# Optimization experiments

Hardware: AMD Instinct MI355X
Metric: run time of the kernel (lower is better)

## Reference

```python
import jax, jax.numpy as jnp
import numpy as np

N = 100000   # nodes
E = 800000   # edges
IN = 128     # input features
HID = 128    # hidden channels (= trans out_channels, heads=1)
OUT = 64     # output classes
EPS = 1e-5
ALPHA = 0.5


def _lin(k, fi, fo):
    kw, kb = jax.random.split(k)
    w = jax.random.normal(kw, (fi, fo), jnp.float32) / np.float32(np.sqrt(fi))
    b = jax.random.normal(kb, (fo,), jnp.float32) * 0.01
    return w, b


def setup_inputs() -> dict:
    key = jax.random.key(0)
    k = jax.random.split(key, 12)
    x = jax.random.normal(k[0], (N, IN), jnp.float32)
    edge_index = jax.random.randint(k[1], (2, E), 0, N)
    edge_type = jax.random.randint(k[2], (E,), 0, 2)
    edge_weight = jax.random.uniform(k[3], (E,), jnp.float32)
    t_fc_w, t_fc_b = _lin(k[4], IN, HID)
    wq, wq_b = _lin(k[5], HID, HID)
    wk, wk_b = _lin(k[6], HID, HID)
    wv, wv_b = _lin(k[7], HID, HID)
    g_fc_w, g_fc_b = _lin(k[8], IN, HID)
    g_w1, g_b1 = _lin(k[9], HID, HID)
    g_w2, g_b2 = _lin(k[10], HID, HID)
    out_w, out_b = _lin(k[11], 2 * HID, OUT)
    ones = jnp.ones((HID,), jnp.float32)
    zeros = jnp.zeros((HID,), jnp.float32)
    return dict(
        x=x, edge_weight=edge_weight,
        t_fc_w=t_fc_w, t_fc_b=t_fc_b, t_ln0_g=ones, t_ln0_b=zeros,
        wq=wq, wq_b=wq_b, wk=wk, wk_b=wk_b, wv=wv, wv_b=wv_b,
        t_ln1_g=ones, t_ln1_b=zeros,
        g_fc_w=g_fc_w, g_fc_b=g_fc_b,
        bn0_g=ones, bn0_b=zeros, bn0_m=zeros, bn0_v=ones,
        g_w1=g_w1, g_b1=g_b1, bn1_g=ones, bn1_b=zeros, bn1_m=zeros, bn1_v=ones,
        g_w2=g_w2, g_b2=g_b2, bn2_g=ones, bn2_b=zeros, bn2_m=zeros, bn2_v=ones,
        out_w=out_w, out_b=out_b,
        edge_index=edge_index, edge_type=edge_type,
    )


def _ln(x, g, b):
    m = x.mean(-1, keepdims=True)
    v = ((x - m) ** 2).mean(-1, keepdims=True)
    return (x - m) / jnp.sqrt(v + EPS) * g + b


def _bn(x, g, b, m, v):  # eval-mode BatchNorm1d (running stats)
    return (x - m) / jnp.sqrt(v + EPS) * g + b


def _full_attn(q, k, v):
    # q:[N,H,M] k:[L,H,M] v:[L,H,D]; global (Frobenius) norm as in torch.norm(qs, p=2)
    q = q / jnp.linalg.norm(q)
    k = k / jnp.linalg.norm(k)
    n = q.shape[0]
    kvs = jnp.einsum('lhm,lhd->hmd', k, v)
    num = jnp.einsum('nhm,hmd->nhd', q, kvs) + n * v
    ksum = k.sum(0)  # [H,M]
    denom = jnp.einsum('nhm,hm->nh', q, ksum)[..., None] + n
    return num / denom


def _hetero(x, row, col, ew, mask, W, b):
    # degree over edges of this type, normalized SpMM: out[col] += val * x[row]
    d = jax.ops.segment_sum(mask.astype(jnp.float32), col, num_segments=N)
    val = ew / jnp.sqrt(d[col] * d[row])
    val = jnp.where(mask, jnp.nan_to_num(val, nan=0.0, posinf=0.0, neginf=0.0), 0.0)
    agg = jax.ops.segment_sum(val[:, None] * x[row], col, num_segments=N)
    return agg @ W + b


def reference(x, edge_weight, t_fc_w, t_fc_b, t_ln0_g, t_ln0_b, wq, wq_b, wk, wk_b,
              wv, wv_b, t_ln1_g, t_ln1_b, g_fc_w, g_fc_b, bn0_g, bn0_b, bn0_m, bn0_v,
              g_w1, g_b1, bn1_g, bn1_b, bn1_m, bn1_v, g_w2, g_b2, bn2_g, bn2_b, bn2_m,
              bn2_v, out_w, out_b, edge_index, edge_type):
    relu = jax.nn.relu
    # --- transformer (kernelized global attention) branch ---
    h = relu(_ln(x @ t_fc_w + t_fc_b, t_ln0_g, t_ln0_b))
    q = (h @ wq + wq_b)[:, None, :]   # [N,1,HID]
    kk = (h @ wk + wk_b)[:, None, :]
    vv = (h @ wv + wv_b)[:, None, :]
    z = _full_attn(q, kk, vv).mean(axis=1)
    x_trans = relu(_ln(ALPHA * z + (1.0 - ALPHA) * h, t_ln1_g, t_ln1_b))
    # --- alternating hetero GNN branch ---
    row, col = edge_index[0], edge_index[1]
    g = relu(_bn(x @ g_fc_w + g_fc_b, bn0_g, bn0_b, bn0_m, bn0_v))
    g1 = relu(_bn(_hetero(g, row, col, edge_weight, edge_type == 0, g_w1, g_b1),
                  bn1_g, bn1_b, bn1_m, bn1_v)) + g
    g2 = relu(_bn(_hetero(g1, row, col, edge_weight, edge_type == 1, g_w2, g_b2),
                  bn2_g, bn2_b, bn2_m, bn2_v)) + g1
    return jnp.tanh(jnp.concatenate([x_trans, g2], axis=1) @ out_w + out_b)
```

## Files before the change

kernel.cpp:

```cpp
#include <hip/hip_runtime.h>
#include <cmath>

#define EPSF 1e-5f

typedef __bf16 bfx8 __attribute__((ext_vector_type(8)));
typedef float  f32x4 __attribute__((ext_vector_type(4)));

__device__ __forceinline__ float4 ld4(const float* p){ return *(const float4*)p; }
__device__ __forceinline__ unsigned f2bf(float f){
    unsigned u = __builtin_bit_cast(unsigned, f);
    return (u + 0x7FFFu + ((u >> 16) & 1u)) >> 16;
}
__device__ __forceinline__ float bf2f(unsigned u){
    return __builtin_bit_cast(float, u << 16);
}
__device__ __forceinline__ bfx8 lds_ld(const char* p){ return *(const bfx8*)p; }
__device__ __forceinline__ unsigned short bf16u(float f){ return (unsigned short)f2bf(f); }

__global__ __launch_bounds__(256)
void wconv_all(const float* __restrict__ s0, const float* __restrict__ s1,
               const float* __restrict__ s2, const float* __restrict__ s3,
               const float* __restrict__ s4, const float* __restrict__ s5,
               unsigned short* __restrict__ WT)
{
    int gid   = blockIdx.x*256 + threadIdx.x;
    int seg   = gid >> 11;
    int chunk = gid & 2047;
    int ln    = chunk & 63;
    unsigned short tmp[8];
    if (seg < 5) {
        const float* s = seg==0?s0: seg==1?s1: seg==2?s2: seg==3?s3: s4;
        int nf = chunk >> 8, ks = (chunk >> 6) & 3;
        int c  = nf*16 + (ln & 15);
        int k0 = ks*32 + (ln >> 4)*8;
        #pragma unroll
        for (int j = 0; j < 8; ++j) tmp[j] = bf16u(s[(size_t)(k0+j)*128 + c]);
        *(uint4*)&WT[seg*16384 + chunk*8] = *(uint4*)tmp;
    } else {
        int nf = chunk >> 9, ks = (chunk >> 6) & 7;
        int c  = nf*16 + (ln & 15);
        int k0 = ks*32 + (ln >> 4)*8;
        #pragma unroll
        for (int j = 0; j < 8; ++j) tmp[j] = bf16u(s5[(size_t)(k0+j)*64 + c]);
        *(uint4*)&WT[5*16384 + chunk*8] = *(uint4*)tmp;
    }
}

__global__ __launch_bounds__(256)
void fused_front(const float* __restrict__ x,
                 const unsigned short* __restrict__ wt_tfc,
                 const unsigned short* __restrict__ wt_wv,
                 const unsigned short* __restrict__ wt_gfc,
                 const float* __restrict__ tfcb, const float* __restrict__ ln0g,
                 const float* __restrict__ ln0b, const float* __restrict__ wvb,
                 const float* __restrict__ ln1g, const float* __restrict__ ln1b,
                 const float* __restrict__ gfcb, const float* __restrict__ bn0g,
                 const float* __restrict__ bn0b, const float* __restrict__ bn0m,
                 const float* __restrict__ bn0v,
                 unsigned short* __restrict__ XTb, float* __restrict__ Gf,
                 unsigned short* __restrict__ Gb, int nrows)
{
    __shared__ __align__(16) char lds[81920];
    char*  Ar  = lds;
    char*  WrA = lds + 16384;
    char*  WrB = lds + 49152;
    float* Cst = (float*)WrB;
    const int tid  = threadIdx.x;
    const int row0 = blockIdx.x * 64;
    const int w  = tid >> 6, ln = tid & 63, lr = ln & 15, lg = ln >> 4;
    const int ksw = (lr & 7) << 4;

    #pragma unroll
    for (int i = 0; i < 4; ++i) {
        int c  = tid + i*256, r = c >> 4, k0 = (c & 15)*8;
        uint4 v4 = make_uint4(0,0,0,0);
        if (row0 + r < nrows) {
            float4 f0 = ld4(&x[(size_t)(row0+r)*128 + k0]);
            float4 f1 = ld4(&x[(size_t)(row0+r)*128 + k0 + 4]);
            v4.x = f2bf(f0.x) | (f2bf(f0.y) << 16);
            v4.y = f2bf(f0.z) | (f2bf(f0.w) << 16);
            v4.z = f2bf(f1.x) | (f2bf(f1.y) << 16);
            v4.w = f2bf(f1.z) | (f2bf(f1.w) << 16);
        }
        *(uint4*)&Ar[r*256 + ((k0*2) ^ ((r&7)<<4))] = v4;
    }
    #pragma unroll
    for (int i = 0; i < 8; ++i) {
        int c = tid + i*256;
        *(uint4*)&WrA[c*16] = *(const uint4*)&wt_tfc[c*8];
    }
    #pragma unroll
    for (int i = 0; i < 8; ++i) {
        int c = tid + i*256;
        *(uint4*)&WrB[c*16] = *(const uint4*)&wt_gfc[c*8];
    }
    __syncthreads();

    const char* Abase = &Ar[(w*16 + lr)*256];
    f32x4 acc[8];
    float h[8][4];

    #pragma unroll
    for (int nf = 0; nf < 8; ++nf) acc[nf] = (f32x4){0.f,0.f,0.f,0.f};
    #pragma unroll
    for (int ks = 0; ks < 4; ++ks) {
        int kb = ks*64 + lg*16;
        bfx8 a = lds_ld(Abase + (kb ^ ksw));
        #pragma unroll
        for (int nf = 0; nf < 8; ++nf) {
            bfx8 b = lds_ld(&WrA[(nf*4+ks)*1024 + ln*16]);
            acc[nf] = __builtin_amdgcn_mfma_f32_16x16x32_bf16(a, b, acc[nf], 0, 0, 0);
        }
    }
    {
        float gl[8], bl[8];
        #pragma unroll
        for (int nf = 0; nf < 8; ++nf) {
            int c = nf*16 + lr;
            gl[nf] = ln0g[c]; bl[nf] = ln0b[c];
            float bb = tfcb[c];
            #pragma unroll
            for (int i = 0; i < 4; ++i) h[nf][i] = acc[nf][i] + bb;
        }
        #pragma unroll
        for (int i = 0; i < 4; ++i) {
            float s = 0.f, s2 = 0.f;
            #pragma unroll
            for (int nf = 0; nf < 8; ++nf) { s += h[nf][i]; s2 += h[nf][i]*h[nf][i]; }
            #pragma unroll
            for (int m = 1; m < 16; m <<= 1) { s += __shfl_xor(s, m); s2 += __shfl_xor(s2, m); }
            float mean = s * (1.f/128.f);
            float inv  = rsqrtf(s2 * (1.f/128.f) - mean*mean + EPSF);
            #pragma unroll
            for (int nf = 0; nf < 8; ++nf)
                h[nf][i] = fmaxf((h[nf][i]-mean)*inv*gl[nf] + bl[nf], 0.f);
        }
    }
    #pragma unroll
    for (int nf = 0; nf < 8; ++nf) acc[nf] = (f32x4){0.f,0.f,0.f,0.f};
    #pragma unroll
    for (int ks = 0; ks < 4; ++ks) {
        int kb = ks*64 + lg*16;
        bfx8 a = lds_ld(Abase + (kb ^ ksw));
        #pragma unroll
        for (int nf = 0; nf < 8; ++nf) {
            bfx8 b = lds_ld(&WrB[(nf*4+ks)*1024 + ln*16]);
            acc[nf] = __builtin_amdgcn_mfma_f32_16x16x32_bf16(a, b, acc[nf], 0, 0, 0);
        }
    }
    #pragma unroll
    for (int nf = 0; nf < 8; ++nf) {
        int c = nf*16 + lr;
        float sc = bn0g[c] * rsqrtf(bn0v[c] + EPSF);
        float sh = bn0b[c] - bn0m[c]*sc;
        float bb = gfcb[c];
        #pragma unroll
        for (int i = 0; i < 4; ++i)
            acc[nf][i] = fmaxf((acc[nf][i] + bb)*sc + sh, 0.f);
    }
    __syncthreads();

    #pragma unroll
    for (int nf = 0; nf < 8; ++nf) {
        int c = nf*16 + lr;
        #pragma unroll
        for (int i = 0; i < 4; ++i) {
            int r = w*16 + lg*4 + i;
            Cst[r*128 + c] = acc[nf][i];
            *(unsigned short*)&Ar[(r*256 + c*2) ^ ((r&7)<<4)] = bf16u(h[nf][i]);
        }
    }
    #pragma unroll
    for (int i = 0; i < 8; ++i) {
        int c = tid + i*256;
        *(uint4*)&WrA[c*16] = *(const uint4*)&wt_wv[c*8];
    }
    __syncthreads();

    #pragma unroll
    for (int i = 0; i < 8; ++i) {
        int c = tid + i*256, r = c >> 5, k4 = (c & 31)*4;
        if (row0 + r < nrows) {
            f32x4 v = *(f32x4*)&Cst[r*128 + k4];
            *(f32x4*)&Gf[(size_t)(row0+r)*128 + k4] = v;
            uint2 pk;
            pk.x = f2bf(v[0]) | (f2bf(v[1]) << 16);
            pk.y = f2bf(v[2]) | (f2bf(v[3]) << 16);
            *(uint2*)&Gb[(size_t)(row0+r)*128 + k4] = pk;
        }
    }
    #pragma unroll
    for (int nf = 0; nf < 8; ++nf) acc[nf] = (f32x4){0.f,0.f,0.f,0.f};
    #pragma unroll
    for (int ks = 0; ks < 4; ++ks) {
        int kb = ks*64 + lg*16;
        bfx8 a = lds_ld(Abase + (kb ^ ksw));
        #pragma unroll
        for (int nf = 0; nf < 8; ++nf) {
            bfx8 b = lds_ld(&WrA[(nf*4+ks)*1024 + ln*16]);
            acc[nf] = __builtin_amdgcn_mfma_f32_16x16x32_bf16(a, b, acc[nf], 0, 0, 0);
        }
    }
    {
        float gl[8], bl[8];
        #pragma unroll
        for (int nf = 0; nf < 8; ++nf) {
            int c = nf*16 + lr;
            gl[nf] = ln1g[c]; bl[nf] = ln1b[c];
            float bb = wvb[c];
            #pragma unroll
            for (int i = 0; i < 4; ++i)
                h[nf][i] = 0.5f*(acc[nf][i] + bb) + 0.5f*h[nf][i];
        }
        #pragma unroll
        for (int i = 0; i < 4; ++i) {
            float s = 0.f, s2 = 0.f;
            #pragma unroll
            for (int nf = 0; nf < 8; ++nf) { s += h[nf][i]; s2 += h[nf][i]*h[nf][i]; }
            #pragma unroll
            for (int m = 1; m < 16; m <<= 1) { s += __shfl_xor(s, m); s2 += __shfl_xor(s2, m); }
            float mean = s * (1.f/128.f);
            float inv  = rsqrtf(s2 * (1.f/128.f) - mean*mean + EPSF);
            #pragma unroll
            for (int nf = 0; nf < 8; ++nf)
                h[nf][i] = fmaxf((h[nf][i]-mean)*inv*gl[nf] + bl[nf], 0.f);
        }
    }
    __syncthreads();

    #pragma unroll
    for (int nf = 0; nf < 8; ++nf) {
        int c = nf*16 + lr;
        #pragma unroll
        for (int i = 0; i < 4; ++i)
            Cst[(w*16 + lg*4 + i)*128 + c] = h[nf][i];
    }
    __syncthreads();
    #pragma unroll
    for (int i = 0; i < 8; ++i) {
        int c = tid + i*256, r = c >> 5, k4 = (c & 31)*4;
        if (row0 + r < nrows) {
            f32x4 v = *(f32x4*)&Cst[r*128 + k4];
            uint2 pk;
            pk.x = f2bf(v[0]) | (f2bf(v[1]) << 16);
            pk.y = f2bf(v[2]) | (f2bf(v[3]) << 16);
            *(uint2*)&XTb[(size_t)(row0+r)*128 + k4] = pk;
        }
    }
}

__global__ __launch_bounds__(256)
void mgemm(const unsigned short* __restrict__ Ab16, const unsigned short* __restrict__ WTf,
           const float* __restrict__ bias, float* __restrict__ Cf,
           unsigned short* __restrict__ Cb, int nrows,
           const float* __restrict__ p0, const float* __restrict__ p1,
           const float* __restrict__ p2, const float* __restrict__ p3,
           const float* __restrict__ resid)
{
    __shared__ __align__(16) char lds[50176];
    char*  Ar  = lds;
    char*  Wr  = lds + 16384;
    float* Cst = (float*)Wr;
    const int tid  = threadIdx.x;
    const int row0 = blockIdx.x * 64;
    const int w  = tid >> 6, ln = tid & 63, lr = ln & 15, lg = ln >> 4;
    const int ksw = (lr & 7) << 4;

    #pragma unroll
    for (int i = 0; i < 4; ++i) {
        int c  = tid + i*256, r = c >> 4, k0 = (c & 15)*8;
        uint4 v = make_uint4(0,0,0,0);
        if (row0 + r < nrows)
            v = *(const uint4*)&Ab16[(size_t)(row0+r)*128 + k0];
        *(uint4*)&Ar[r*256 + ((k0*2) ^ ((r&7)<<4))] = v;
    }
    #pragma unroll
    for (int i = 0; i < 8; ++i) {
        int c = tid + i*256;
        *(uint4*)&Wr[c*16] = *(const uint4*)&WTf[c*8];
    }
    __syncthreads();

    const char* Abase = &Ar[(w*16 + lr)*256];
    f32x4 acc[8];
    #pragma unroll
    for (int nf = 0; nf < 8; ++nf) acc[nf] = (f32x4){0.f,0.f,0.f,0.f};
    #pragma unroll
    for (int ks = 0; ks < 4; ++ks) {
        int kb = ks*64 + lg*16;
        bfx8 a = lds_ld(Abase + (kb ^ ksw));
        #pragma unroll
        for (int nf = 0; nf < 8; ++nf) {
            bfx8 b = lds_ld(&Wr[(nf*4+ks)*1024 + ln*16]);
            acc[nf] = __builtin_amdgcn_mfma_f32_16x16x32_bf16(a, b, acc[nf], 0, 0, 0);
        }
    }

    float t[8][4];
    #pragma unroll
    for (int nf = 0; nf < 8; ++nf) {
        int c = nf*16 + lr;
        float sc = p0[c] * rsqrtf(p3[c] + EPSF);
        float sh = p1[c] - p2[c]*sc;
        float bb = bias[c];
        #pragma unroll
        for (int i = 0; i < 4; ++i)
            t[nf][i] = fmaxf((acc[nf][i] + bb)*sc + sh, 0.f);
    }

    __syncthreads();
    #pragma unroll
    for (int nf = 0; nf < 8; ++nf)
        #pragma unroll
        for (int i = 0; i < 4; ++i)
            Cst[(w*16 + lg*4 + i)*132 + nf*16 + lr] = t[nf][i];
    __syncthreads();
    #pragma unroll
    for (int i = 0; i < 8; ++i) {
        int c = tid + i*256, r = c >> 5, c4 = (c & 31)*4;
        if (row0 + r >= nrows) continue;
        f32x4 v = *(f32x4*)&Cst[r*132 + c4];
        float4 rr = ld4(resid + (size_t)(row0+r)*128 + c4);
        v.x += rr.x; v.y += rr.y; v.z += rr.z; v.w += rr.w;
        *(f32x4*)&Cf[(size_t)(row0+r)*128 + c4] = v;
        uint2 pk;
        pk.x = f2bf(v.x) | (f2bf(v.y) << 16);
        pk.y = f2bf(v.z) | (f2bf(v.w) << 16);
        *(uint2*)&Cb[(size_t)(row0+r)*128 + c4] = pk;
    }
}

__global__ __launch_bounds__(256)
void mgemm_out(const unsigned short* __restrict__ Ab16,
               const unsigned short* __restrict__ WTf,
               const float* __restrict__ bias,
               const float* __restrict__ p0, const float* __restrict__ p1,
               const float* __restrict__ p2, const float* __restrict__ p3,
               const float* __restrict__ resid,
               const unsigned short* __restrict__ XTb,
               const unsigned short* __restrict__ WToutf,
               const float* __restrict__ outB,
               float* __restrict__ out, int nrows)
{
    __shared__ __align__(16) char lds[65536];
    char* Ar  = lds;
    char* Wg  = lds + 16384;
    char* WrX = lds + 16384;
    char* WrO = lds + 32768;
    const int tid  = threadIdx.x;
    const int row0 = blockIdx.x * 64;
    const int w  = tid >> 6, ln = tid & 63, lr = ln & 15, lg = ln >> 4;
    const int ksw = (lr & 7) << 4;

    #pragma unroll
    for (int i = 0; i < 4; ++i) {
        int c  = tid + i*256, r = c >> 4, k0 = (c & 15)*8;
        uint4 v = make_uint4(0,0,0,0);
        if (row0 + r < nrows)
            v = *(const uint4*)&Ab16[(size_t)(row0+r)*128 + k0];
        *(uint4*)&Ar[r*256 + ((k0*2) ^ ((r&7)<<4))] = v;
    }
    #pragma unroll
    for (int i = 0; i < 8; ++i) {
        int c = tid + i*256;
        *(uint4*)&Wg[c*16] = *(const uint4*)&WTf[c*8];
    }
    __syncthreads();

    const char* Abase = &Ar[(w*16 + lr)*256];
    f32x4 acc[8];
    #pragma unroll
    for (int nf = 0; nf < 8; ++nf) acc[nf] = (f32x4){0.f,0.f,0.f,0.f};
    #pragma unroll
    for (int ks = 0; ks < 4; ++ks) {
        int kb = ks*64 + lg*16;
        bfx8 a = lds_ld(Abase + (kb ^ ksw));
        #pragma unroll
        for (int nf = 0; nf < 8; ++nf) {
            bfx8 b = lds_ld(&Wg[(nf*4+ks)*1024 + ln*16]);
            acc[nf] = __builtin_amdgcn_mfma_f32_16x16x32_bf16(a, b, acc[nf], 0, 0, 0);
        }
    }
    float t[8][4];
    #pragma unroll
    for (int nf = 0; nf < 8; ++nf) {
        int c = nf*16 + lr;
        float sc = p0[c] * rsqrtf(p3[c] + EPSF);
        float sh = p1[c] - p2[c]*sc;
        float bb = bias[c];
        #pragma unroll
        for (int i = 0; i < 4; ++i) {
            int r = row0 + w*16 + lg*4 + i;
            float rv = (r < nrows) ? resid[(size_t)r*128 + c] : 0.f;
            t[nf][i] = fmaxf((acc[nf][i] + bb)*sc + sh, 0.f) + rv;
        }
    }
    __syncthreads();

    #pragma unroll
    for (int nf = 0; nf < 8; ++nf) {
        int c = nf*16 + lr;
        #pragma unroll
        for (int i = 0; i < 4; ++i) {
            int r = w*16 + lg*4 + i;
            *(unsigned short*)&Ar[(r*256 + c*2) ^ ((r&7)<<4)] = bf16u(t[nf][i]);
        }
    }
    #pragma unroll
    for (int i = 0; i < 4; ++i) {
        int c  = tid + i*256, r = c >> 4, k0 = (c & 15)*8;
        uint4 v = make_uint4(0,0,0,0);
        if (row0 + r < nrows)
            v = *(const uint4*)&XTb[(size_t)(row0+r)*128 + k0];
        *(uint4*)&WrX[r*256 + ((k0*2) ^ ((r&7)<<4))] = v;
    }
    #pragma unroll
    for (int i = 0; i < 8; ++i) {
        int c = tid + i*256;
        *(uint4*)&WrO[c*16] = *(const uint4*)&WToutf[c*8];
    }
    __syncthreads();

    f32x4 acc2[4];
    #pragma unroll
    for (int nf = 0; nf < 4; ++nf) acc2[nf] = (f32x4){0.f,0.f,0.f,0.f};
    const char* Xbase = &WrX[(w*16 + lr)*256];
    #pragma unroll
    for (int ks = 0; ks < 8; ++ks) {
        int kb = (ks & 3)*64 + lg*16;
        bfx8 a = (ks < 4) ? lds_ld(Xbase + (kb ^ ksw))
                          : lds_ld(Abase + (kb ^ ksw));
        #pragma unroll
        for (int nf = 0; nf < 4; ++nf) {
            bfx8 b = lds_ld(&WrO[(nf*8+ks)*1024 + ln*16]);
            acc2[nf] = __builtin_amdgcn_mfma_f32_16x16x32_bf16(a, b, acc2[nf], 0, 0, 0);
        }
    }
    #pragma unroll
    for (int nf = 0; nf < 4; ++nf) {
        float bb = outB[nf*16 + lr];
        #pragma unroll
        for (int i = 0; i < 4; ++i) {
            int r = row0 + w*16 + lg*4 + i;
            if (r < nrows)
                out[(size_t)r*64 + nf*16 + lr] = tanhf(acc2[nf][i] + bb);
        }
    }
}

__global__ __launch_bounds__(256)
void edge_hist(const int* __restrict__ col, const int* __restrict__ et,
               int* __restrict__ cnt, int* __restrict__ ePos, int n, int ne)
{
    int e = blockIdx.x*256 + threadIdx.x;
    if (e >= ne) return;
    int pos = atomicAdd(&cnt[et[e]*n + col[e]], 1);
    ePos[e] = pos;
}

__global__ __launch_bounds__(1024)
void scan_block(const int* __restrict__ cnt, int2* __restrict__ co,
                int* __restrict__ bsum, int n)
{
    __shared__ int s[1024];
    const int t = threadIdx.x;
    const int i = blockIdx.x*1024 + t;
    int v = (i < n) ? cnt[i] : 0;
    s[t] = v;
    __syncthreads();
    #pragma unroll
    for (int d = 1; d < 1024; d <<= 1) {
        int u = (t >= d) ? s[t-d] : 0;
        __syncthreads();
        s[t] += u;
        __syncthreads();
    }
    if (i < n) co[i] = make_int2(v, s[t] - v);
    if (t == 1023) bsum[blockIdx.x] = s[1023];
}

__global__ __launch_bounds__(256)
void scan_bsums(int* __restrict__ bsum, int nb)
{
    __shared__ int s[256];
    const int t = threadIdx.x;
    int v = (t < nb) ? bsum[t] : 0;
    s[t] = v;
    __syncthreads();
    #pragma unroll
    for (int d = 1; d < 256; d <<= 1) {
        int u = (t >= d) ? s[t-d] : 0;
        __syncthreads();
        s[t] += u;
        __syncthreads();
    }
    if (t < nb) bsum[t] = s[t] - v;
}

__global__ __launch_bounds__(256)
void edge_fill(const int* __restrict__ row_idx, const int* __restrict__ col_idx,
               const int* __restrict__ et, const float* __restrict__ ew,
               const int2* __restrict__ co, const int* __restrict__ bsum,
               const int* __restrict__ ePos,
               uint2* __restrict__ ePack, int n, int ne)
{
    int e = blockIdx.x*256 + threadIdx.x;
    if (e >= ne) return;
    int t = et[e], c = col_idx[e], r = row_idx[e];
    int ic = t*n + c;
    int2 qc = co[ic];
    int2 qr = co[t*n + r];
    int idx = qc.y + bsum[ic >> 10] + ePos[e];
    int p = qc.x * qr.x;
    float val = (p > 0) ? ew[e] * rsqrtf((float)p) : 0.f;
    ePack[idx] = make_uint2((unsigned)r, __builtin_bit_cast(unsigned, val));
}

__global__ __launch_bounds__(256)
void hetero_gather(const unsigned short* __restrict__ Gb,
                   const uint2* __restrict__ ePack,
                   const int2* __restrict__ co, const int* __restrict__ bsum,
                   int t0, unsigned short* __restrict__ AGGb, int n)
{
    int node = blockIdx.x*4 + (threadIdx.x >> 6);
    if (node >= n) return;
    const int lane = threadIdx.x & 63;
    const int gi   = t0 + node;
    int2 q = co[gi];
    const int base = q.y + bsum[gi >> 10];
    const int m = q.x;
    float ax = 0.f, ay = 0.f;
    int i = 0;
    for (; i + 3 < m; i += 4) {
        uint2 q0 = ePack[base+i];
        uint2 q1 = ePack[base+i+1];
        uint2 q2 = ePack[base+i+2];
        uint2 q3 = ePack[base+i+3];
        unsigned g0 = *(const unsigned*)&Gb[(size_t)q0.x*128 + lane*2];
        unsigned g1 = *(const unsigned*)&Gb[(size_t)q1.x*128 + lane*2];
        unsigned g2 = *(const unsigned*)&Gb[(size_t)q2.x*128 + lane*2];
        unsigned g3 = *(const unsigned*)&Gb[(size_t)q3.x*128 + lane*2];
        float v0 = __builtin_bit_cast(float, q0.y);
        float v1 = __builtin_bit_cast(float, q1.y);
        float v2 = __builtin_bit_cast(float, q2.y);
        float v3 = __builtin_bit_cast(float, q3.y);
        ax += v0*bf2f(g0 & 0xffff) + v1*bf2f(g1 & 0xffff)
            + v2*bf2f(g2 & 0xffff) + v3*bf2f(g3 & 0xffff);
        ay += v0*bf2f(g0 >> 16)    + v1*bf2f(g1 >> 16)
            + v2*bf2f(g2 >> 16)    + v3*bf2f(g3 >> 16);
    }
    for (; i < m; ++i) {
        uint2 q0 = ePack[base+i];
        unsigned g0 = *(const unsigned*)&Gb[(size_t)q0.x*128 + lane*2];
        float v0 = __builtin_bit_cast(float, q0.y);
        ax += v0*bf2f(g0 & 0xffff);
        ay += v0*bf2f(g0 >> 16);
    }
    unsigned pk = f2bf(ax) | (f2bf(ay) << 16);
    *(unsigned*)&AGGb[(size_t)node*128 + lane*2] = pk;
}

extern "C" void kernel_launch(void* const* d_in, const int* in_sizes, int n_in,
                              void* d_out, int out_size, void* d_ws, size_t ws_size,
                              hipStream_t stream)
{
    const float* x      = (const float*)d_in[0];
    const float* ew     = (const float*)d_in[1];
    const float* t_fc_w = (const float*)d_in[2];
    const float* t_fc_b = (const float*)d_in[3];
    const float* ln0g   = (const float*)d_in[4];
    const float* ln0b   = (const float*)d_in[5];
    const float* wvw    = (const float*)d_in[10];
    const float* wvb    = (const float*)d_in[11];
    const float* ln1g   = (const float*)d_in[12];
    const float* ln1b   = (const float*)d_in[13];
    const float* gfcw   = (const float*)d_in[14];
    const float* gfcb   = (const float*)d_in[15];
    const float* bn0g   = (const float*)d_in[16];
    const float* bn0b   = (const float*)d_in[17];
    const float* bn0m   = (const float*)d_in[18];
    const float* bn0v   = (const float*)d_in[19];
    const float* gw1    = (const float*)d_in[20];
    const float* gb1    = (const float*)d_in[21];
    const float* bn1g   = (const float*)d_in[22];
    const float* bn1b   = (const float*)d_in[23];
    const float* bn1m   = (const float*)d_in[24];
    const float* bn1v   = (const float*)d_in[25];
    const float* gw2    = (const float*)d_in[26];
    const float* gb2    = (const float*)d_in[27];
    const float* bn2g   = (const float*)d_in[28];
    const float* bn2b   = (const float*)d_in[29];
    const float* bn2m   = (const float*)d_in[30];
    const float* bn2v   = (const float*)d_in[31];
    const float* outw   = (const float*)d_in[32];
    const float* outb   = (const float*)d_in[33];
    const int*   ei     = (const int*)d_in[34];
    const int*   et     = (const int*)d_in[35];

    const int N = 100000, E = 800000;
    const size_t NF = (size_t)N*128;
    float* F1 = (float*)d_ws;
    float* F2 = F1 + NF;
    unsigned short* B1 = (unsigned short*)(F2 + NF);
    unsigned short* B3 = B1 + NF;
    unsigned short* B4 = B3 + NF;
    unsigned short* WT = B4 + NF;
    unsigned short* wt_tfc = WT;
    unsigned short* wt_wv  = WT + 16384;
    unsigned short* wt_gfc = WT + 2*16384;
    unsigned short* wt_g1  = WT + 3*16384;
    unsigned short* wt_g2  = WT + 4*16384;
    unsigned short* wt_out = WT + 5*16384;
    int*   cnt    = (int*)(WT + 6*16384);
    int2*  co     = (int2*)(cnt + 2*N);
    int*   ePos   = (int*)(co + 2*N);
    uint2* ePack  = (uint2*)(ePos + E);
    int*   bsum   = (int*)(ePack + E);

    dim3 blk(256);
    const int nb64 = (N + 63) / 64;
    const int* row_idx = ei;
    const int* col_idx = ei + E;
    const int nscan = 2*N;
    const int nsb = (nscan + 1023) / 1024;

    hipMemsetAsync(cnt, 0, 2*(size_t)N*sizeof(int), stream);
    edge_hist<<<(E + 255)/256, blk, 0, stream>>>(col_idx, et, cnt, ePos, N, E);
    scan_block<<<nsb, 1024, 0, stream>>>(cnt, co, bsum, nscan);
    scan_bsums<<<1, 256, 0, stream>>>(bsum, nsb);
    edge_fill<<<(E + 255)/256, blk, 0, stream>>>(row_idx, col_idx, et, ew,
                                                 co, bsum, ePos, ePack, N, E);

    wconv_all<<<48, blk, 0, stream>>>(t_fc_w, wvw, gfcw, gw1, gw2, outw, WT);

    fused_front<<<nb64, blk, 0, stream>>>(x, wt_tfc, wt_wv, wt_gfc,
        t_fc_b, ln0g, ln0b, wvb, ln1g, ln1b,
        gfcb, bn0g, bn0b, bn0m, bn0v, B4, F2, B3, N);

    hetero_gather<<<(N + 3)/4, blk, 0, stream>>>(B3, ePack, co, bsum, 0, B1, N);
    mgemm<<<nb64, blk, 0, stream>>>(B1, wt_g1, gb1, F1, B3, N,
                                    bn1g, bn1b, bn1m, bn1v, F2);
    hetero_gather<<<(N + 3)/4, blk, 0, stream>>>(B3, ePack, co, bsum, N, B1, N);
    mgemm_out<<<nb64, blk, 0, stream>>>(B1, wt_g2, gb2,
        bn2g, bn2b, bn2m, bn2v, F1, B4, wt_out, outb, (float*)d_out, N);
}
```

Measured before the change: 277.0 us.

## Make fused_front persistent with resident weights and double-buffered x prefetch

Turns the front GEMM kernel into a persistent kernel with a 256-block grid that loops over 64-row tiles. All three weight matrices are loaded into LDS once per block, and the next tile's x rows are prefetched into registers and written into a second A buffer while the current tile computes. Outputs are now written straight from registers instead of being staged through LDS, which gives up coalesced vector stores for scattered 2- and 4-byte stores. The 128KB LDS footprint limits each CU to one block, and a 256-block grid may leave some CUs idle.

```diff
diff --git a/kernel.cpp b/kernel.cpp
--- a/kernel.cpp
+++ b/kernel.cpp
@@ -58,194 +58,203 @@
                  const float* __restrict__ bn0b, const float* __restrict__ bn0m,
                  const float* __restrict__ bn0v,
                  unsigned short* __restrict__ XTb, float* __restrict__ Gf,
-                 unsigned short* __restrict__ Gb, int nrows)
-{
-    __shared__ __align__(16) char lds[81920];
-    char*  Ar  = lds;
-    char*  WrA = lds + 16384;
-    char*  WrB = lds + 49152;
-    float* Cst = (float*)WrB;
-    const int tid  = threadIdx.x;
-    const int row0 = blockIdx.x * 64;
-    const int w  = tid >> 6, ln = tid & 63, lr = ln & 15, lg = ln >> 4;
+                 unsigned short* __restrict__ Gb, int nrows, int ntiles)
+{
+    __shared__ __align__(16) char lds[131072];
+    char* ArA = lds;
+    char* ArB = lds + 16384;
+    char* Wt  = lds + 32768;
+    char* Wg  = lds + 65536;
+    char* Wv  = lds + 98304;
+    const int tid = threadIdx.x;
+    const int w = tid >> 6, ln = tid & 63, lr = ln & 15, lg = ln >> 4;
     const int ksw = (lr & 7) << 4;
 
-    #pragma unroll
-    for (int i = 0; i < 4; ++i) {
-        int c  = tid + i*256, r = c >> 4, k0 = (c & 15)*8;
-        uint4 v4 = make_uint4(0,0,0,0);
-        if (row0 + r < nrows) {
-            float4 f0 = ld4(&x[(size_t)(row0+r)*128 + k0]);
-            float4 f1 = ld4(&x[(size_t)(row0+r)*128 + k0 + 4]);
-            v4.x = f2bf(f0.x) | (f2bf(f0.y) << 16);
-            v4.y = f2bf(f0.z) | (f2bf(f0.w) << 16);
-            v4.z = f2bf(f1.x) | (f2bf(f1.y) << 16);
-            v4.w = f2bf(f1.z) | (f2bf(f1.w) << 16);
-        }
-        *(uint4*)&Ar[r*256 + ((k0*2) ^ ((r&7)<<4))] = v4;
-    }
     #pragma unroll
     for (int i = 0; i < 8; ++i) {
         int c = tid + i*256;
-        *(uint4*)&WrA[c*16] = *(const uint4*)&wt_tfc[c*8];
-    }
-    #pragma unroll
-    for (int i = 0; i < 8; ++i) {
-        int c = tid + i*256;
-        *(uint4*)&WrB[c*16] = *(const uint4*)&wt_gfc[c*8];
-    }
-    __syncthreads();
-
-    const char* Abase = &Ar[(w*16 + lr)*256];
-    f32x4 acc[8];
-    float h[8][4];
-
-    #pragma unroll
-    for (int nf = 0; nf < 8; ++nf) acc[nf] = (f32x4){0.f,0.f,0.f,0.f};
-    #pragma unroll
-    for (int ks = 0; ks < 4; ++ks) {
-        int kb = ks*64 + lg*16;
-        bfx8 a = lds_ld(Abase + (kb ^ ksw));
-        #pragma unroll
-        for (int nf = 0; nf < 8; ++nf) {
-            bfx8 b = lds_ld(&WrA[(nf*4+ks)*1024 + ln*16]);
-            acc[nf] = __builtin_amdgcn_mfma_f32_16x16x32_bf16(a, b, acc[nf], 0, 0, 0);
-        }
+        *(uint4*)&Wt[c*16] = *(const uint4*)&wt_tfc[c*8];
+        *(uint4*)&Wg[c*16] = *(const uint4*)&wt_gfc[c*8];
+        *(uint4*)&Wv[c*16] = *(const uint4*)&wt_wv[c*8];
     }
     {
-        float gl[8], bl[8];
+        int t0 = blockIdx.x;
+        #pragma unroll
+        for (int i = 0; i < 4; ++i) {
+            int c = tid + i*256, r = c >> 4, k0 = (c & 15)*8;
+            int rr = t0*64 + r;
+            uint4 v4 = make_uint4(0,0,0,0);
+            if (t0 < ntiles && rr < nrows) {
+                float4 f0 = ld4(&x[(size_t)rr*128 + k0]);
+                float4 f1 = ld4(&x[(size_t)rr*128 + k0 + 4]);
+                v4.x = f2bf(f0.x) | (f2bf(f0.y) << 16);
+                v4.y = f2bf(f0.z) | (f2bf(f0.w) << 16);
+                v4.z = f2bf(f1.x) | (f2bf(f1.y) << 16);
+                v4.w = f2bf(f1.z) | (f2bf(f1.w) << 16);
+            }
+            *(uint4*)&ArA[r*256 + ((k0*2) ^ ((r&7)<<4))] = v4;
+        }
+    }
+    __syncthreads();
+
+    bool par = false;
+    for (int tile = blockIdx.x; tile < ntiles; tile += gridDim.x) {
+        char* Acur = par ? ArB : ArA;
+        char* Anxt = par ? ArA : ArB;
+        const int  row0 = tile*64;
+        const int  nxt  = tile + gridDim.x;
+        const bool havenxt = (nxt < ntiles);
+        const char* Abase = &Acur[(w*16 + lr)*256];
+
+        float4 xa[4], xb[4];
+        if (havenxt) {
+            #pragma unroll
+            for (int i = 0; i < 4; ++i) {
+                int c = tid + i*256, r = c >> 4, k0 = (c & 15)*8;
+                int rr = nxt*64 + r;
+                if (rr < nrows) {
+                    xa[i] = ld4(&x[(size_t)rr*128 + k0]);
+                    xb[i] = ld4(&x[(size_t)rr*128 + k0 + 4]);
+                } else {
+                    xa[i] = make_float4(0.f,0.f,0.f,0.f);
+                    xb[i] = make_float4(0.f,0.f,0.f,0.f);
+                }
+            }
+        }
+
+        f32x4 acc[8];
+        float h[8][4];
+
+        #pragma unroll
+        for (int nf = 0; nf < 8; ++nf) acc[nf] = (f32x4){0.f,0.f,0.f,0.f};
+        #pragma unroll
+        for (int ks = 0; ks < 4; ++ks) {
+            int kb = ks*64 + lg*16;
+            bfx8 a = lds_ld(Abase + (kb ^ ksw));
+            #pragma unroll
+            for (int nf = 0; nf < 8; ++nf) {
+                bfx8 b = lds_ld(&Wt[(nf*4+ks)*1024 + ln*16]);
+                acc[nf] = __builtin_amdgcn_mfma_f32_16x16x32_bf16(a, b, acc[nf], 0, 0, 0);
+            }
+        }
+        {
+            float gl[8], bl[8];
+            #pragma unroll
+            for (int nf = 0; nf < 8; ++nf) {
+                int c = nf*16 + lr;
+                gl[nf] = ln0g[c]; bl[nf] = ln0b[c];
+                float bb = tfcb[c];
+                #pragma unroll
+                for (int i = 0; i < 4; ++i) h[nf][i] = acc[nf][i] + bb;
+            }
+            #pragma unroll
+            for (int i = 0; i < 4; ++i) {
+                float s = 0.f, s2 = 0.f;
+                #pragma unroll
+                for (int nf = 0; nf < 8; ++nf) { s += h[nf][i]; s2 += h[nf][i]*h[nf][i]; }
+                #pragma unroll
+                for (int m = 1; m < 16; m <<= 1) { s += __shfl_xor(s, m); s2 += __shfl_xor(s2, m); }
+                float mean = s * (1.f/128.f);
+                float inv  = rsqrtf(s2 * (1.f/128.f) - mean*mean + EPSF);
+                #pragma unroll
+                for (int nf = 0; nf < 8; ++nf)
+                    h[nf][i] = fmaxf((h[nf][i]-mean)*inv*gl[nf] + bl[nf], 0.f);
+            }
+        }
+        #pragma unroll
+        for (int nf = 0; nf < 8; ++nf) acc[nf] = (f32x4){0.f,0.f,0.f,0.f};
+        #pragma unroll
+        for (int ks = 0; ks < 4; ++ks) {
+            int kb = ks*64 + lg*16;
+            bfx8 a = lds_ld(Abase + (kb ^ ksw));
+            #pragma unroll
+            for (int nf = 0; nf < 8; ++nf) {
+                bfx8 b = lds_ld(&Wg[(nf*4+ks)*1024 + ln*16]);
+                acc[nf] = __builtin_amdgcn_mfma_f32_16x16x32_bf16(a, b, acc[nf], 0, 0, 0);
+            }
+        }
         #pragma unroll
         for (int nf = 0; nf < 8; ++nf) {
             int c = nf*16 + lr;
-            gl[nf] = ln0g[c]; bl[nf] = ln0b[c];
-            float bb = tfcb[c];
-            #pragma unroll
-            for (int i = 0; i < 4; ++i) h[nf][i] = acc[nf][i] + bb;
-        }
-        #pragma unroll
-        for (int i = 0; i < 4; ++i) {
-            float s = 0.f, s2 = 0.f;
-            #pragma unroll
-            for (int nf = 0; nf < 8; ++nf) { s += h[nf][i]; s2 += h[nf][i]*h[nf][i]; }
-            #pragma unroll
-            for (int m = 1; m < 16; m <<= 1) { s += __shfl_xor(s, m); s2 += __shfl_xor(s2, m); }
-            float mean = s * (1.f/128.f);
-            float inv  = rsqrtf(s2 * (1.f/128.f) - mean*mean + EPSF);
-            #pragma unroll
-            for (int nf = 0; nf < 8; ++nf)
-                h[nf][i] = fmaxf((h[nf][i]-mean)*inv*gl[nf] + bl[nf], 0.f);
-        }
-    }
-    #pragma unroll
-    for (int nf = 0; nf < 8; ++nf) acc[nf] = (f32x4){0.f,0.f,0.f,0.f};
-    #pragma unroll
-    for (int ks = 0; ks < 4; ++ks) {
-        int kb = ks*64 + lg*16;
-        bfx8 a = lds_ld(Abase + (kb ^ ksw));
-        #pragma unroll
-        for (int nf = 0; nf < 8; ++nf) {
-            bfx8 b = lds_ld(&WrB[(nf*4+ks)*1024 + ln*16]);
-            acc[nf] = __builtin_amdgcn_mfma_f32_16x16x32_bf16(a, b, acc[nf], 0, 0, 0);
-        }
-    }
-    #pragma unroll
-    for (int nf = 0; nf < 8; ++nf) {
-        int c = nf*16 + lr;
-        float sc = bn0g[c] * rsqrtf(bn0v[c] + EPSF);
-        float sh = bn0b[c] - bn0m[c]*sc;
-        float bb = gfcb[c];
-        #pragma unroll
-        for (int i = 0; i < 4; ++i)
-            acc[nf][i] = fmaxf((acc[nf][i] + bb)*sc + sh, 0.f);
-    }
-    __syncthreads();
-
-    #pragma unroll
-    for (int nf = 0; nf < 8; ++nf) {
-        int c = nf*16 + lr;
-        #pragma unroll
-        for (int i = 0; i < 4; ++i) {
-            int r = w*16 + lg*4 + i;
-            Cst[r*128 + c] = acc[nf][i];
-            *(unsigned short*)&Ar[(r*256 + c*2) ^ ((r&7)<<4)] = bf16u(h[nf][i]);
-        }
-    }
-    #pragma unroll
-    for (int i = 0; i < 8; ++i) {
-        int c = tid + i*256;
-        *(uint4*)&WrA[c*16] = *(const uint4*)&wt_wv[c*8];
-    }
-    __syncthreads();
-
-    #pragma unroll
-    for (int i = 0; i < 8; ++i) {
-        int c = tid + i*256, r = c >> 5, k4 = (c & 31)*4;
-        if (row0 + r < nrows) {
-            f32x4 v = *(f32x4*)&Cst[r*128 + k4];
-            *(f32x4*)&Gf[(size_t)(row0+r)*128 + k4] = v;
-            uint2 pk;
-            pk.x = f2bf(v[0]) | (f2bf(v[1]) << 16);
-            pk.y = f2bf(v[2]) | (f2bf(v[3]) << 16);
-            *(uint2*)&Gb[(size_t)(row0+r)*128 + k4] = pk;
-        }
-    }
-    #pragma unroll
-    for (int nf = 0; nf < 8; ++nf) acc[nf] = (f32x4){0.f,0.f,0.f,0.f};
-    #pragma unroll
-    for (int ks = 0; ks < 4; ++ks) {
-        int kb = ks*64 + lg*16;
-        bfx8 a = lds_ld(Abase + (kb ^ ksw));
-        #pragma unroll
-        for (int nf = 0; nf < 8; ++nf) {
-            bfx8 b = lds_ld(&WrA[(nf*4+ks)*1024 + ln*16]);
-            acc[nf] = __builtin_amdgcn_mfma_f32_16x16x32_bf16(a, b, acc[nf], 0, 0, 0);
-        }
-    }
-    {
-        float gl[8], bl[8];
+            float sc = bn0g[c] * rsqrtf(bn0v[c] + EPSF);
+            float sh = bn0b[c] - bn0m[c]*sc;
+            float bb = gfcb[c];
+            #pragma unroll
+            for (int i = 0; i < 4; ++i) {
+                int r = row0 + w*16 + lg*4 + i;
+                if (r < nrows) {
+                    float v = fmaxf((acc[nf][i] + bb)*sc + sh, 0.f);
+                    Gf[(size_t)r*128 + c] = v;
+                    Gb[(size_t)r*128 + c] = bf16u(v);
+                }
+            }
+        }
+        if (havenxt) {
+            #pragma unroll
+            for (int i = 0; i < 4; ++i) {
+                int c = tid + i*256, r = c >> 4, k0 = (c & 15)*8;
+                uint4 v4;
+                v4.x = f2bf(xa[i].x) | (f2bf(xa[i].y) << 16);
+                v4.y = f2bf(xa[i].z) | (f2bf(xa[i].w) << 16);
+                v4.z = f2bf(xb[i].x) | (f2bf(xb[i].y) << 16);
+                v4.w = f2bf(xb[i].z) | (f2bf(xb[i].w) << 16);
+                *(uint4*)&Anxt[r*256 + ((k0*2) ^ ((r&7)<<4))] = v4;
+            }
+        }
+        __syncthreads();
         #pragma unroll
         for (int nf = 0; nf < 8; ++nf) {
             int c = nf*16 + lr;
-            gl[nf] = ln1g[c]; bl[nf] = ln1b[c];
-            float bb = wvb[c];
-            #pragma unroll
-            for (int i = 0; i < 4; ++i)
-                h[nf][i] = 0.5f*(acc[nf][i] + bb) + 0.5f*h[nf][i];
-        }
-        #pragma unroll
-        for (int i = 0; i < 4; ++i) {
-            float s = 0.f, s2 = 0.f;
-            #pragma unroll
-            for (int nf = 0; nf < 8; ++nf) { s += h[nf][i]; s2 += h[nf][i]*h[nf][i]; }
-            #pragma unroll
-            for (int m = 1; m < 16; m <<= 1) { s += __shfl_xor(s, m); s2 += __shfl_xor(s2, m); }
-            float mean = s * (1.f/128.f);
-            float inv  = rsqrtf(s2 * (1.f/128.f) - mean*mean + EPSF);
-            #pragma unroll
-            for (int nf = 0; nf < 8; ++nf)
-                h[nf][i] = fmaxf((h[nf][i]-mean)*inv*gl[nf] + bl[nf], 0.f);
-        }
-    }
-    __syncthreads();
-
-    #pragma unroll
-    for (int nf = 0; nf < 8; ++nf) {
-        int c = nf*16 + lr;
-        #pragma unroll
-        for (int i = 0; i < 4; ++i)
-            Cst[(w*16 + lg*4 + i)*128 + c] = h[nf][i];
-    }
-    __syncthreads();
-    #pragma unroll
-    for (int i = 0; i < 8; ++i) {
-        int c = tid + i*256, r = c >> 5, k4 = (c & 31)*4;
-        if (row0 + r < nrows) {
-            f32x4 v = *(f32x4*)&Cst[r*128 + k4];
-            uint2 pk;
-            pk.x = f2bf(v[0]) | (f2bf(v[1]) << 16);
-            pk.y = f2bf(v[2]) | (f2bf(v[3]) << 16);
-            *(uint2*)&XTb[(size_t)(row0+r)*128 + k4] = pk;
-        }
+            #pragma unroll
+            for (int i = 0; i < 4; ++i) {
+                int r = w*16 + lg*4 + i;
+                *(unsigned short*)&Acur[(r*256 + c*2) ^ ((r&7)<<4)] = bf16u(h[nf][i]);
+            }
+        }
+        __syncthreads();
+        #pragma unroll
+        for (int nf = 0; nf < 8; ++nf) acc[nf] = (f32x4){0.f,0.f,0.f,0.f};
+        #pragma unroll
+        for (int ks = 0; ks < 4; ++ks) {
+            int kb = ks*64 + lg*16;
+            bfx8 a = lds_ld(Abase + (kb ^ ksw));
+            #pragma unroll
+            for (int nf = 0; nf < 8; ++nf) {
+                bfx8 b = lds_ld(&Wv[(nf*4+ks)*1024 + ln*16]);
+                acc[nf] = __builtin_amdgcn_mfma_f32_16x16x32_bf16(a, b, acc[nf], 0, 0, 0);
+            }
+        }
+        {
+            float gl[8], bl[8];
+            #pragma unroll
+            for (int nf = 0; nf < 8; ++nf) {
+                int c = nf*16 + lr;
+                gl[nf] = ln1g[c]; bl[nf] = ln1b[c];
+                float bb = wvb[c];
+                #pragma unroll
+                for (int i = 0; i < 4; ++i)
+                    h[nf][i] = 0.5f*(acc[nf][i] + bb) + 0.5f*h[nf][i];
+            }
+            #pragma unroll
+            for (int i = 0; i < 4; ++i) {
+                float s = 0.f, s2 = 0.f;
+                #pragma unroll
+                for (int nf = 0; nf < 8; ++nf) { s += h[nf][i]; s2 += h[nf][i]*h[nf][i]; }
+                #pragma unroll
+                for (int m = 1; m < 16; m <<= 1) { s += __shfl_xor(s, m); s2 += __shfl_xor(s2, m); }
+                float mean = s * (1.f/128.f);
+                float inv  = rsqrtf(s2 * (1.f/128.f) - mean*mean + EPSF);
+                int rbase = row0 + w*16 + lg*4 + i;
+                #pragma unroll
+                for (int nf = 0; nf < 8; ++nf) {
+                    float v = fmaxf((h[nf][i]-mean)*inv*gl[nf] + bl[nf], 0.f);
+                    if (rbase < nrows)
+                        XTb[(size_t)rbase*128 + nf*16 + lr] = bf16u(v);
+                }
+            }
+        }
+        __syncthreads();
+        par = !par;
     }
 }
 
@@ -633,9 +642,9 @@
 
     wconv_all<<<48, blk, 0, stream>>>(t_fc_w, wvw, gfcw, gw1, gw2, outw, WT);
 
-    fused_front<<<nb64, blk, 0, stream>>>(x, wt_tfc, wt_wv, wt_gfc,
+    fused_front<<<256, blk, 0, stream>>>(x, wt_tfc, wt_wv, wt_gfc,
         t_fc_b, ln0g, ln0b, wvb, ln1g, ln1b,
-        gfcb, bn0g, bn0b, bn0m, bn0v, B4, F2, B3, N);
+        gfcb, bn0g, bn0b, bn0m, bn0v, B4, F2, B3, N, nb64);
 
     hetero_gather<<<(N + 3)/4, blk, 0, stream>>>(B3, ePack, co, bsum, 0, B1, N);
     mgemm<<<nb64, blk, 0, stream>>>(B1, wt_g1, gb1, F1, B3, N,
```

Result: slower. 290.7 us (+4.9%).
